# Kernel optimization log

Hardware: AMD Instinct MI355X
Metric: run time of the kernel (lower is better)

The kernel has to match this reference:

```python
import jax, jax.numpy as jnp
import numpy as np

NUM_CLUSTERS = 8
NUM_ITERS = 3
SIM_TEMP = 10.0
EPS = 1e-12  # F.normalize default eps


def _l2norm(x):
    n = jnp.linalg.norm(x, axis=-1, keepdims=True)
    return x / jnp.maximum(n, EPS)


def setup_inputs() -> dict:
    key = jax.random.key(0)
    ks = jax.random.split(key, 5)
    B, P, C = 8, 16384, 256
    F_p = jax.random.normal(ks[0], (B, P, C), dtype=jnp.float32)
    scale = 1.0 / np.sqrt(C)
    proj_w = jax.random.normal(ks[1], (C, C), dtype=jnp.float32) * scale
    proj_b = jax.random.normal(ks[2], (C,), dtype=jnp.float32) * scale
    refine_w = jax.random.normal(ks[3], (C, C), dtype=jnp.float32) * scale
    refine_b = jax.random.normal(ks[4], (C,), dtype=jnp.float32) * scale
    return {"F_p": F_p, "proj_w": proj_w, "proj_b": proj_b,
            "refine_w": refine_w, "refine_b": refine_b}


def reference(F_p, proj_w, proj_b, refine_w, refine_b):
    B, P, C = F_p.shape
    c = min(NUM_CLUSTERS, P)
    nodes = F_p @ proj_w.T + proj_b  # (B, P, C)
    # initial centers: evenly spaced node indices (torch.linspace(...).long())
    idx = jnp.asarray(np.linspace(0, P - 1, c).astype(np.int64))
    centers = nodes[:, idx, :]  # (B, c, C)
    nodes_norm = _l2norm(nodes)
    for _ in range(NUM_ITERS):
        sim = jnp.einsum('bpc,bkc->bpk', nodes_norm, _l2norm(centers))
        assignments = jnp.argmax(sim, axis=-1)  # (B, P)
        onehot = jax.nn.one_hot(assignments, c, dtype=nodes.dtype)  # (B, P, c)
        counts = jnp.maximum(onehot.sum(axis=1), 1.0)  # (B, c), clamp(min=1)
        # masked mean per cluster == segment mean via one-hot contraction
        centers = jnp.einsum('bpk,bpc->bkc', onehot, nodes) / counts[..., None]
    sim = jnp.einsum('bpc,bkc->bpk', nodes_norm, _l2norm(centers))
    weights = jax.nn.softmax(sim * SIM_TEMP, axis=-1)  # (B, P, c)
    clustered = jnp.einsum('bpk,bkc->bpc', weights, centers)
    return (clustered + F_p) @ refine_w.T + refine_b
```

## Files before the change

### kernel.cpp

```cpp
#include <hip/hip_runtime.h>
#include <hip/hip_bf16.h>
#include <cmath>

#define BB 8
#define PP 16384
#define CC 256
#define NCLUS 8
#define BPROWS (BB*PP)

typedef unsigned int uint;
typedef unsigned short ushort;
typedef __bf16 bf16x8 __attribute__((ext_vector_type(8)));
typedef float f32x16 __attribute__((ext_vector_type(16)));

__device__ __forceinline__ float bflo(uint u){ return __uint_as_float(u << 16); }
__device__ __forceinline__ float bfhi(uint u){ return __uint_as_float(u & 0xffff0000u); }
__device__ __forceinline__ ushort f2bf(float x){ __hip_bfloat16 h = __float2bfloat16(x); return *(ushort*)&h; }
__device__ __forceinline__ uint pk2(float a, float b){ return (uint)f2bf(a) | ((uint)f2bf(b) << 16); }

__global__ __launch_bounds__(256) void wcvt(const float* __restrict__ Wp,
    const float* __restrict__ Wr, ushort* __restrict__ Wpb, ushort* __restrict__ Wrb) {
  int i = blockIdx.x*256 + threadIdx.x;
  float4 a = *(const float4*)(Wp + (size_t)i*4);
  float4 b = *(const float4*)(Wr + (size_t)i*4);
  *(uint2*)(Wpb + (size_t)i*4) = make_uint2(pk2(a.x,a.y), pk2(a.z,a.w));
  *(uint2*)(Wrb + (size_t)i*4) = make_uint2(pk2(b.x,b.y), pk2(b.z,b.w));
}

template<bool PROJ>
__global__ __launch_bounds__(512) void gemm_bf16(const void* __restrict__ Av,
    const ushort* __restrict__ Wb, const float* __restrict__ bias,
    void* __restrict__ Dv, float* __restrict__ rnorm,
    const float* __restrict__ W8, const float* __restrict__ CR,
    ushort* __restrict__ fbf) {
  __shared__ __align__(16) char AlB[128*64*2];
  __shared__ __align__(16) char WlB[256*64*2];
  __shared__ float rnp[128][4];
  const int t  = threadIdx.x;
  const int p0 = blockIdx.x * 128;
  const int lane = t & 63;
  const int w  = t >> 6;
  const int wr = w >> 2, wc = w & 3;

  int aoff[2]; size_t agb[2];
  const ushort* asrc[2]; char* adst[2];
  #pragma unroll
  for (int i = 0; i < 2; ++i) {
    int S = i*512 + t, row = S >> 3, sc = S & 7;
    if constexpr (PROJ) {
      aoff[i] = row*128 + ((sc*16) ^ ((row & 7) << 4));
      agb[i]  = (size_t)(p0 + row)*CC + sc*8;
    } else {
      asrc[i] = (const ushort*)Av + (size_t)(p0 + row)*CC + ((sc ^ (row & 7)) << 3);
      adst[i] = AlB + (size_t)S*16;
    }
  }
  const ushort* wsrc[4]; char* wdst[4];
  #pragma unroll
  for (int i = 0; i < 4; ++i) {
    int S = i*512 + t, row = S >> 3, sc = S & 7;
    wsrc[i] = Wb + (size_t)row*CC + ((sc ^ (row & 7)) << 3);
    wdst[i] = WlB + (size_t)S*16;
  }
  const int arow = (wr << 6) + (lane & 31);
  const int brow = (wc << 6) + (lane & 31);
  const int kb0  = (lane >> 5) << 4;

  uint4 ra[2];
  auto LOADA = [&](int ks) {
    const float* A = (const float*)Av;
    #pragma unroll
    for (int i = 0; i < 2; ++i) {
      float4 v0 = *(const float4*)(A + agb[i] + ks*64);
      float4 v1 = *(const float4*)(A + agb[i] + ks*64 + 4);
      ra[i] = make_uint4(pk2(v0.x,v0.y), pk2(v0.z,v0.w), pk2(v1.x,v1.y), pk2(v1.z,v1.w));
    }
  };
  auto WRITEA = [&](int ks) {
    #pragma unroll
    for (int i = 0; i < 2; ++i) {
      *(uint4*)(AlB + aoff[i]) = ra[i];
      *(uint4*)(fbf + agb[i] + ks*64) = ra[i];
    }
  };
  auto STAGEA_LDS = [&](int ks) {
    #pragma unroll
    for (int i = 0; i < 2; ++i)
      __builtin_amdgcn_global_load_lds(
          (const __attribute__((address_space(1))) uint*)(asrc[i] + ks*64),
          (__attribute__((address_space(3))) uint*)adst[i], 16, 0, 0);
  };
  auto STAGEW = [&](int ks) {
    #pragma unroll
    for (int i = 0; i < 4; ++i)
      __builtin_amdgcn_global_load_lds(
          (const __attribute__((address_space(1))) uint*)(wsrc[i] + ks*64),
          (__attribute__((address_space(3))) uint*)wdst[i], 16, 0, 0);
  };

  f32x16 acc[2][2];
  #pragma unroll
  for (int fm = 0; fm < 2; ++fm)
    #pragma unroll
    for (int fn = 0; fn < 2; ++fn)
      #pragma unroll
      for (int r = 0; r < 16; ++r) acc[fm][fn][r] = 0.0f;

  if constexpr (PROJ) {
    LOADA(0); STAGEW(0); WRITEA(0);
  } else {
    STAGEA_LDS(0); STAGEW(0);
  }
  __syncthreads();

  #pragma unroll
  for (int ks = 0; ks < 4; ++ks) {
    if constexpr (PROJ) { if (ks < 3) LOADA(ks+1); }
    bf16x8 af[2][4], bg[2][4];
    #pragma unroll
    for (int fm = 0; fm < 2; ++fm)
      #pragma unroll
      for (int kq = 0; kq < 4; ++kq) {
        int row = arow + (fm << 5);
        int off = row*128 + (((kq << 5) + kb0) ^ ((row & 7) << 4));
        af[fm][kq] = *(const bf16x8*)(AlB + off);
      }
    #pragma unroll
    for (int fn = 0; fn < 2; ++fn)
      #pragma unroll
      for (int kq = 0; kq < 4; ++kq) {
        int row = brow + (fn << 5);
        int off = row*128 + (((kq << 5) + kb0) ^ ((row & 7) << 4));
        bg[fn][kq] = *(const bf16x8*)(WlB + off);
      }
    #pragma unroll
    for (int kq = 0; kq < 4; ++kq)
      #pragma unroll
      for (int fm = 0; fm < 2; ++fm)
        #pragma unroll
        for (int fn = 0; fn < 2; ++fn)
          acc[fm][fn] = __builtin_amdgcn_mfma_f32_32x32x16_bf16(
              af[fm][kq], bg[fn][kq], acc[fm][fn], 0, 0, 0);
    if (ks < 3) {
      __syncthreads();
      if constexpr (PROJ) { STAGEW(ks+1); WRITEA(ks+1); }
      else               { STAGEA_LDS(ks+1); STAGEW(ks+1); }
      __syncthreads();
    }
  }

  const int colb = (wc << 6) + (lane & 31);
  const float b0 = bias[colb], b1 = bias[colb + 32];
  float cr0[8], cr1[8];
  if constexpr (!PROJ) {
    const float* crb = CR + (size_t)(blockIdx.x >> 7)*NCLUS*CC;
    #pragma unroll
    for (int k = 0; k < 8; ++k) { cr0[k] = crb[k*CC + colb]; cr1[k] = crb[k*CC + colb + 32]; }
  }
  #pragma unroll
  for (int fm = 0; fm < 2; ++fm) {
    float rs[16];
    #pragma unroll
    for (int r = 0; r < 16; ++r) {
      int rowin = (r & 3) + ((r >> 2) << 3) + ((lane >> 5) << 2);
      size_t grow = (size_t)(p0 + (wr << 6) + (fm << 5) + rowin);
      float v0 = acc[fm][0][r] + b0;
      float v1 = acc[fm][1][r] + b1;
      if constexpr (PROJ) {
        ushort* D = (ushort*)Dv;
        D[grow*CC + colb]      = f2bf(v0);
        D[grow*CC + colb + 32] = f2bf(v1);
        rs[r] = v0*v0 + v1*v1;
      } else {
        float4 ua = *(const float4*)(W8 + grow*8);
        float4 ub = *(const float4*)(W8 + grow*8 + 4);
        v0 += ua.x*cr0[0] + ua.y*cr0[1] + ua.z*cr0[2] + ua.w*cr0[3]
            + ub.x*cr0[4] + ub.y*cr0[5] + ub.z*cr0[6] + ub.w*cr0[7];
        v1 += ua.x*cr1[0] + ua.y*cr1[1] + ua.z*cr1[2] + ua.w*cr1[3]
            + ub.x*cr1[4] + ub.y*cr1[5] + ub.z*cr1[6] + ub.w*cr1[7];
        float* D = (float*)Dv;
        D[grow*CC + colb]      = v0;
        D[grow*CC + colb + 32] = v1;
      }
    }
    if constexpr (PROJ) {
      #pragma unroll
      for (int m = 1; m < 32; m <<= 1)
        #pragma unroll
        for (int r = 0; r < 16; ++r) rs[r] += __shfl_xor(rs[r], m);
      if ((lane & 31) == 0) {
        #pragma unroll
        for (int r = 0; r < 16; ++r) {
          int rowin = (r & 3) + ((r >> 2) << 3) + ((lane >> 5) << 2);
          rnp[(wr << 6) + (fm << 5) + rowin][wc] = rs[r];
        }
      }
    }
  }
  if constexpr (PROJ) {
    __syncthreads();
    if (t < 128) {
      float s = rnp[t][0] + rnp[t][1] + rnp[t][2] + rnp[t][3];
      rnorm[p0 + t] = 1.0f / fmaxf(sqrtf(s), 1e-12f);
    }
  }
}

__global__ __launch_bounds__(256) void centers_init(const ushort* __restrict__ nbf,
    float* __restrict__ centers, ushort* __restrict__ cnormbf,
    float* __restrict__ accs, float* __restrict__ counts) {
  const int idxs[8] = {0, 2340, 4680, 7021, 9361, 11702, 14042, 16383};
  const int row = blockIdx.x;
  const int b = row >> 3, k = row & 7;
  const int t = threadIdx.x;
  float c = __uint_as_float(((uint)nbf[((size_t)b*PP + idxs[k])*CC + t]) << 16);
  centers[(size_t)row*CC + t] = c;
  float s2 = c*c;
  #pragma unroll
  for (int o = 32; o; o >>= 1) s2 += __shfl_xor(s2, o);
  __shared__ float ps[4];
  if ((t & 63) == 0) ps[t >> 6] = s2;
  __syncthreads();
  float tot = ps[0] + ps[1] + ps[2] + ps[3];
  cnormbf[(size_t)row*CC + t] = f2bf(c * (1.0f / fmaxf(sqrtf(tot), 1e-12f)));
  #pragma unroll
  for (int s = 0; s < 8; ++s) accs[((size_t)s*64 + row)*CC + t] = 0.0f;
  if (t == 0) counts[row] = 0.0f;
}

__global__ __launch_bounds__(256) void centers_finalize(float* __restrict__ accs,
    float* __restrict__ counts, ushort* __restrict__ cnormbf, float* __restrict__ centers) {
  const int row = blockIdx.x;
  const int t = threadIdx.x;
  float v = 0.0f;
  #pragma unroll
  for (int s = 0; s < 8; ++s) {
    v += accs[((size_t)s*64 + row)*CC + t];
    accs[((size_t)s*64 + row)*CC + t] = 0.0f;
  }
  float cnt = fmaxf(counts[row], 1.0f);
  float c = v / cnt;
  centers[(size_t)row*CC + t] = c;
  float s2 = c*c;
  #pragma unroll
  for (int o = 32; o; o >>= 1) s2 += __shfl_xor(s2, o);
  __shared__ float ps[4];
  if ((t & 63) == 0) ps[t >> 6] = s2;
  __syncthreads();
  float tot = ps[0] + ps[1] + ps[2] + ps[3];
  cnormbf[(size_t)row*CC + t] = f2bf(c * (1.0f / fmaxf(sqrtf(tot), 1e-12f)));
  if (t == 0) counts[row] = 0.0f;
}

__global__ __launch_bounds__(256) void cr8_compute(const float* __restrict__ centers,
    const float* __restrict__ Wr, float* __restrict__ CR) {
  __shared__ float cenL[CC];
  const int row = blockIdx.x;
  const int t = threadIdx.x;
  cenL[t] = centers[(size_t)row*CC + t];
  __syncthreads();
  float a = 0.0f;
  const float* wrow = Wr + (size_t)t*CC;
  #pragma unroll 4
  for (int j = 0; j < CC; j += 4) {
    float4 wv = *(const float4*)(wrow + j);
    float4 cv = *(const float4*)&cenL[j];
    a += cv.x*wv.x + cv.y*wv.y + cv.z*wv.z + cv.w*wv.w;
  }
  CR[(size_t)row*CC + t] = a;
}

__device__ __forceinline__ void sims_mfma(const ushort* __restrict__ nb_base,
    const ushort* __restrict__ cnb, int lane, float* s) {
  const int pcol = lane & 31;
  const int kb   = (lane >> 5) << 3;
  const ushort* arow = cnb + (size_t)(pcol & 7)*CC + kb;
  const ushort* brow = nb_base + (size_t)pcol*CC + kb;
  const bool azero = pcol >= 8;
  bf16x8 z;
  #pragma unroll
  for (int j = 0; j < 8; ++j) z[j] = (__bf16)0.0f;
  f32x16 acc;
  #pragma unroll
  for (int r = 0; r < 16; ++r) acc[r] = 0.0f;
  #pragma unroll
  for (int st = 0; st < 16; ++st) {
    bf16x8 af = *(const bf16x8*)(arow + st*16);
    if (azero) af = z;
    bf16x8 bg = *(const bf16x8*)(brow + st*16);
    acc = __builtin_amdgcn_mfma_f32_32x32x16_bf16(af, bg, acc, 0, 0, 0);
  }
  float sh[4];
  #pragma unroll
  for (int r = 0; r < 4; ++r) sh[r] = __shfl_xor(acc[r], 32);
  const bool hi = lane >= 32;
  #pragma unroll
  for (int r = 0; r < 4; ++r) {
    s[r]     = hi ? sh[r]  : acc[r];
    s[r + 4] = hi ? acc[r] : sh[r];
  }
}

__global__ __launch_bounds__(256) void assign_mfma(const ushort* __restrict__ nbf,
    const ushort* __restrict__ cnormbf, float* __restrict__ accs, float* __restrict__ counts) {
  __shared__ int assignL[128];
  __shared__ int cntL[NCLUS];
  const int t = threadIdx.x;
  const int wave = t >> 6, lane = t & 63;
  const int b = blockIdx.x >> 7;
  if (t < NCLUS) cntL[t] = 0;
  __syncthreads();
  const size_t p0w = (size_t)blockIdx.x*128 + wave*32;
  float s[8];
  sims_mfma(nbf + p0w*CC, cnormbf + (size_t)b*NCLUS*CC, lane, s);
  if (lane < 32) {
    int best = 0; float bs = s[0];
    #pragma unroll
    for (int k = 1; k < 8; ++k) if (s[k] > bs) { bs = s[k]; best = k; }
    assignL[wave*32 + lane] = best;
    atomicAdd(&cntL[best], 1);
  }
  __syncthreads();
  float a[8] = {0,0,0,0,0,0,0,0};
  const ushort* base = nbf + (size_t)blockIdx.x*128*CC;
  #pragma unroll 4
  for (int i = 0; i < 128; ++i) {
    int asg = __builtin_amdgcn_readfirstlane(assignL[i]);
    float v = __uint_as_float(((uint)base[(size_t)i*CC + t]) << 16);
    if      (asg == 0) a[0] += v;
    else if (asg == 1) a[1] += v;
    else if (asg == 2) a[2] += v;
    else if (asg == 3) a[3] += v;
    else if (asg == 4) a[4] += v;
    else if (asg == 5) a[5] += v;
    else if (asg == 6) a[6] += v;
    else               a[7] += v;
  }
  const int slot = blockIdx.x & 7;
  float* dst = accs + ((size_t)slot*BB + b)*NCLUS*CC;
  #pragma unroll
  for (int k = 0; k < 8; ++k) atomicAdd(&dst[k*CC + t], a[k]);
  if (t < NCLUS) atomicAdd(&counts[b*NCLUS + t], (float)cntL[t]);
}

__global__ __launch_bounds__(256) void fuse_w8(const ushort* __restrict__ nbf,
    const ushort* __restrict__ cnormbf, const float* __restrict__ rnorm,
    float* __restrict__ W8) {
  const int t = threadIdx.x;
  const int wave = t >> 6, lane = t & 63;
  const int b = blockIdx.x >> 7;
  const size_t p0w = (size_t)blockIdx.x*128 + wave*32;
  float s[8];
  sims_mfma(nbf + p0w*CC, cnormbf + (size_t)b*NCLUS*CC, lane, s);
  const int pcol = lane & 31;
  const float rn10 = rnorm[p0w + pcol] * 10.0f;
  float m = -1e30f;
  #pragma unroll
  for (int k = 0; k < 8; ++k) { s[k] *= rn10; m = fmaxf(m, s[k]); }
  float wgt[8], sw = 0.0f;
  #pragma unroll
  for (int k = 0; k < 8; ++k) { wgt[k] = __expf(s[k] - m); sw += wgt[k]; }
  const float inv = 1.0f / sw;
  if (lane < 32) {
    float* wp = W8 + (p0w + pcol)*8;
    *(float4*)(wp)     = make_float4(wgt[0]*inv, wgt[1]*inv, wgt[2]*inv, wgt[3]*inv);
    *(float4*)(wp + 4) = make_float4(wgt[4]*inv, wgt[5]*inv, wgt[6]*inv, wgt[7]*inv);
  }
}

extern "C" void kernel_launch(void* const* d_in, const int* in_sizes, int n_in,
                              void* d_out, int out_size, void* d_ws, size_t ws_size,
                              hipStream_t stream) {
  const float* F_p      = (const float*)d_in[0];
  const float* proj_w   = (const float*)d_in[1];
  const float* proj_b   = (const float*)d_in[2];
  const float* refine_w = (const float*)d_in[3];
  const float* refine_b = (const float*)d_in[4];
  float* out = (float*)d_out;

  char* ws = (char*)d_ws;
  ushort* nbf    = (ushort*)ws;
  ushort* fbf    = (ushort*)(ws + (size_t)BPROWS*CC*2);
  float*  rnorm  = (float*)(ws + (size_t)BPROWS*CC*4);
  float*  centers= rnorm + BPROWS;
  float*  accs   = centers + BB*NCLUS*CC;
  float*  counts = accs + 8*BB*NCLUS*CC;
  float*  CR     = counts + 64;
  ushort* cnormbf= (ushort*)(CR + BB*NCLUS*CC);
  ushort* Wpb    = cnormbf + BB*NCLUS*CC;
  ushort* Wrb    = Wpb + CC*CC;
  float*  W8     = (float*)(Wrb + CC*CC);

  wcvt<<<64, 256, 0, stream>>>(proj_w, refine_w, Wpb, Wrb);
  gemm_bf16<true><<<1024, 512, 0, stream>>>(F_p, Wpb, proj_b, nbf, rnorm, nullptr, nullptr, fbf);
  centers_init<<<64, 256, 0, stream>>>(nbf, centers, cnormbf, accs, counts);
  for (int it = 0; it < 3; ++it) {
    assign_mfma<<<1024, 256, 0, stream>>>(nbf, cnormbf, accs, counts);
    centers_finalize<<<64, 256, 0, stream>>>(accs, counts, cnormbf, centers);
  }
  fuse_w8<<<1024, 256, 0, stream>>>(nbf, cnormbf, rnorm, W8);
  cr8_compute<<<64, 256, 0, stream>>>(centers, refine_w, CR);
  gemm_bf16<false><<<1024, 512, 0, stream>>>(fbf, Wrb, refine_b, out, nullptr, W8, CR, nullptr);
}
```

Before: 285.0 us.

## Double-buffer A tile in LDS and load weight fragments directly from global

The GEMM kernel stops staging the weight tile in LDS. Each lane now reads its B fragments straight from global memory, relying on the small weight matrix being cache-resident. The A tile is double-buffered so the next k-slice can be prefetched into the alternate buffer while the current one is consumed, which removes one barrier per k-step. The trade-off is more global/L2 traffic for the weights, with uncoalesced per-lane 16-byte reads, in exchange for less LDS use and fewer syncs.

Result: slower. 334.0 us (+17.2%).

```diff
diff --git a/kernel.cpp b/kernel.cpp
--- a/kernel.cpp
+++ b/kernel.cpp
@@ -33,8 +33,7 @@
     void* __restrict__ Dv, float* __restrict__ rnorm,
     const float* __restrict__ W8, const float* __restrict__ CR,
     ushort* __restrict__ fbf) {
-  __shared__ __align__(16) char AlB[128*64*2];
-  __shared__ __align__(16) char WlB[256*64*2];
+  __shared__ __align__(16) char AlB[2][128*64*2];
   __shared__ float rnp[128][4];
   const int t  = threadIdx.x;
   const int p0 = blockIdx.x * 128;
@@ -43,7 +42,7 @@
   const int wr = w >> 2, wc = w & 3;
 
   int aoff[2]; size_t agb[2];
-  const ushort* asrc[2]; char* adst[2];
+  const ushort* asrc[2]; int adoff[2];
   #pragma unroll
   for (int i = 0; i < 2; ++i) {
     int S = i*512 + t, row = S >> 3, sc = S & 7;
@@ -51,20 +50,13 @@
       aoff[i] = row*128 + ((sc*16) ^ ((row & 7) << 4));
       agb[i]  = (size_t)(p0 + row)*CC + sc*8;
     } else {
-      asrc[i] = (const ushort*)Av + (size_t)(p0 + row)*CC + ((sc ^ (row & 7)) << 3);
-      adst[i] = AlB + (size_t)S*16;
-    }
-  }
-  const ushort* wsrc[4]; char* wdst[4];
-  #pragma unroll
-  for (int i = 0; i < 4; ++i) {
-    int S = i*512 + t, row = S >> 3, sc = S & 7;
-    wsrc[i] = Wb + (size_t)row*CC + ((sc ^ (row & 7)) << 3);
-    wdst[i] = WlB + (size_t)S*16;
+      asrc[i]  = (const ushort*)Av + (size_t)(p0 + row)*CC + ((sc ^ (row & 7)) << 3);
+      adoff[i] = S*16;
+    }
   }
   const int arow = (wr << 6) + (lane & 31);
   const int brow = (wc << 6) + (lane & 31);
-  const int kb0  = (lane >> 5) << 4;
+  const ushort* wptr = Wb + (size_t)brow*CC + ((lane >> 5) << 3);
 
   uint4 ra[2];
   auto LOADA = [&](int ks) {
@@ -76,27 +68,20 @@
       ra[i] = make_uint4(pk2(v0.x,v0.y), pk2(v0.z,v0.w), pk2(v1.x,v1.y), pk2(v1.z,v1.w));
     }
   };
-  auto WRITEA = [&](int ks) {
+  auto WRITEA = [&](int ks, char* abuf) {
     #pragma unroll
     for (int i = 0; i < 2; ++i) {
-      *(uint4*)(AlB + aoff[i]) = ra[i];
+      *(uint4*)(abuf + aoff[i]) = ra[i];
       *(uint4*)(fbf + agb[i] + ks*64) = ra[i];
     }
   };
-  auto STAGEA_LDS = [&](int ks) {
+  auto STAGEA = [&](int ks, char* abuf) {
     #pragma unroll
     for (int i = 0; i < 2; ++i)
       __builtin_amdgcn_global_load_lds(
           (const __attribute__((address_space(1))) uint*)(asrc[i] + ks*64),
-          (__attribute__((address_space(3))) uint*)adst[i], 16, 0, 0);
+          (__attribute__((address_space(3))) uint*)(abuf + adoff[i]), 16, 0, 0);
   };
-  auto STAGEW = [&](int ks) {
-    #pragma unroll
-    for (int i = 0; i < 4; ++i)
-      __builtin_amdgcn_global_load_lds(
-          (const __attribute__((address_space(1))) uint*)(wsrc[i] + ks*64),
-          (__attribute__((address_space(3))) uint*)wdst[i], 16, 0, 0);
-  };
 
   f32x16 acc[2][2];
   #pragma unroll
@@ -106,32 +91,32 @@
       #pragma unroll
       for (int r = 0; r < 16; ++r) acc[fm][fn][r] = 0.0f;
 
-  if constexpr (PROJ) {
-    LOADA(0); STAGEW(0); WRITEA(0);
-  } else {
-    STAGEA_LDS(0); STAGEW(0);
-  }
+  if constexpr (PROJ) { LOADA(0); WRITEA(0, AlB[0]); }
+  else                { STAGEA(0, AlB[0]); }
   __syncthreads();
 
   #pragma unroll
   for (int ks = 0; ks < 4; ++ks) {
-    if constexpr (PROJ) { if (ks < 3) LOADA(ks+1); }
-    bf16x8 af[2][4], bg[2][4];
+    char* cur = AlB[ks & 1];
+    char* nxt = AlB[(ks + 1) & 1];
+    if (ks < 3) {
+      if constexpr (PROJ) LOADA(ks + 1);
+      else                STAGEA(ks + 1, nxt);
+    }
+    bf16x8 bg[2][4];
+    #pragma unroll
+    for (int fn = 0; fn < 2; ++fn)
+      #pragma unroll
+      for (int kq = 0; kq < 4; ++kq)
+        bg[fn][kq] = *(const bf16x8*)(wptr + (size_t)fn*32*CC + ks*64 + kq*16);
+    bf16x8 af[2][4];
     #pragma unroll
     for (int fm = 0; fm < 2; ++fm)
       #pragma unroll
       for (int kq = 0; kq < 4; ++kq) {
         int row = arow + (fm << 5);
-        int off = row*128 + (((kq << 5) + kb0) ^ ((row & 7) << 4));
-        af[fm][kq] = *(const bf16x8*)(AlB + off);
-      }
-    #pragma unroll
-    for (int fn = 0; fn < 2; ++fn)
-      #pragma unroll
-      for (int kq = 0; kq < 4; ++kq) {
-        int row = brow + (fn << 5);
-        int off = row*128 + (((kq << 5) + kb0) ^ ((row & 7) << 4));
-        bg[fn][kq] = *(const bf16x8*)(WlB + off);
+        int off = row*128 + (((kq << 5) + ((lane >> 5) << 4)) ^ ((row & 7) << 4));
+        af[fm][kq] = *(const bf16x8*)(cur + off);
       }
     #pragma unroll
     for (int kq = 0; kq < 4; ++kq)
@@ -142,9 +127,7 @@
           acc[fm][fn] = __builtin_amdgcn_mfma_f32_32x32x16_bf16(
               af[fm][kq], bg[fn][kq], acc[fm][fn], 0, 0, 0);
     if (ks < 3) {
-      __syncthreads();
-      if constexpr (PROJ) { STAGEW(ks+1); WRITEA(ks+1); }
-      else               { STAGEA_LDS(ks+1); STAGEW(ks+1); }
+      if constexpr (PROJ) WRITEA(ks + 1, nxt);
       __syncthreads();
     }
   }
```

## Fuse softmax weight computation into refine GEMM and CR into final center update

Applied to the files above, without the earlier changes.

The separate fuse_w8 kernel is removed: the second GEMM now computes the per-row similarity softmax weights in its first four waves during the prologue and keeps them in shared memory, so the W8 buffer is never written to or read from global memory. The cr8_compute kernel is folded into the last centers_finalize launch through a template flag, and the stored float centers buffer is dropped. This removes two launches and a global round trip, but adds extra MFMA and load work to the GEMM prologue, which may delay the main loop.

After: 282.4 us. About the same (-0.9%).

```diff
diff --git a/kernel.cpp b/kernel.cpp
--- a/kernel.cpp
+++ b/kernel.cpp
@@ -14,7 +14,6 @@
 typedef float f32x16 __attribute__((ext_vector_type(16)));
 
 __device__ __forceinline__ float bflo(uint u){ return __uint_as_float(u << 16); }
-__device__ __forceinline__ float bfhi(uint u){ return __uint_as_float(u & 0xffff0000u); }
 __device__ __forceinline__ ushort f2bf(float x){ __hip_bfloat16 h = __float2bfloat16(x); return *(ushort*)&h; }
 __device__ __forceinline__ uint pk2(float a, float b){ return (uint)f2bf(a) | ((uint)f2bf(b) << 16); }
 
@@ -27,15 +26,46 @@
   *(uint2*)(Wrb + (size_t)i*4) = make_uint2(pk2(b.x,b.y), pk2(b.z,b.w));
 }
 
+__device__ __forceinline__ void sims_mfma(const ushort* __restrict__ nb_base,
+    const ushort* __restrict__ cnb, int lane, float* s) {
+  const int pcol = lane & 31;
+  const int kb   = (lane >> 5) << 3;
+  const ushort* arow = cnb + (size_t)(pcol & 7)*CC + kb;
+  const ushort* brow = nb_base + (size_t)pcol*CC + kb;
+  const bool azero = pcol >= 8;
+  bf16x8 z;
+  #pragma unroll
+  for (int j = 0; j < 8; ++j) z[j] = (__bf16)0.0f;
+  f32x16 acc;
+  #pragma unroll
+  for (int r = 0; r < 16; ++r) acc[r] = 0.0f;
+  #pragma unroll
+  for (int st = 0; st < 16; ++st) {
+    bf16x8 af = *(const bf16x8*)(arow + st*16);
+    if (azero) af = z;
+    bf16x8 bg = *(const bf16x8*)(brow + st*16);
+    acc = __builtin_amdgcn_mfma_f32_32x32x16_bf16(af, bg, acc, 0, 0, 0);
+  }
+  float sh[4];
+  #pragma unroll
+  for (int r = 0; r < 4; ++r) sh[r] = __shfl_xor(acc[r], 32);
+  const bool hi = lane >= 32;
+  #pragma unroll
+  for (int r = 0; r < 4; ++r) {
+    s[r]     = hi ? sh[r]  : acc[r];
+    s[r + 4] = hi ? acc[r] : sh[r];
+  }
+}
+
 template<bool PROJ>
 __global__ __launch_bounds__(512) void gemm_bf16(const void* __restrict__ Av,
     const ushort* __restrict__ Wb, const float* __restrict__ bias,
     void* __restrict__ Dv, float* __restrict__ rnorm,
-    const float* __restrict__ W8, const float* __restrict__ CR,
-    ushort* __restrict__ fbf) {
+    const float* __restrict__ CR, ushort* __restrict__ fbf,
+    const ushort* __restrict__ nbf, const ushort* __restrict__ cnormbf) {
   __shared__ __align__(16) char AlB[128*64*2];
   __shared__ __align__(16) char WlB[256*64*2];
-  __shared__ float rnp[128][4];
+  __shared__ __align__(16) float shr8[128][8];
   const int t  = threadIdx.x;
   const int p0 = blockIdx.x * 128;
   const int lane = t & 63;
@@ -83,7 +113,7 @@
       *(uint4*)(fbf + agb[i] + ks*64) = ra[i];
     }
   };
-  auto STAGEA_LDS = [&](int ks) {
+  auto STAGEA = [&](int ks) {
     #pragma unroll
     for (int i = 0; i < 2; ++i)
       __builtin_amdgcn_global_load_lds(
@@ -109,13 +139,32 @@
   if constexpr (PROJ) {
     LOADA(0); STAGEW(0); WRITEA(0);
   } else {
-    STAGEA_LDS(0); STAGEW(0);
+    STAGEA(0); STAGEW(0);
+    if (w < 4) {
+      const size_t p0w = (size_t)p0 + w*32;
+      float s[8];
+      sims_mfma(nbf + p0w*CC, cnormbf + (size_t)(blockIdx.x >> 7)*NCLUS*CC, lane, s);
+      const int pcol = lane & 31;
+      const float rn10 = rnorm[p0w + pcol] * 10.0f;
+      float m = -1e30f;
+      #pragma unroll
+      for (int k = 0; k < 8; ++k) { s[k] *= rn10; m = fmaxf(m, s[k]); }
+      float wgt[8], sw = 0.0f;
+      #pragma unroll
+      for (int k = 0; k < 8; ++k) { wgt[k] = __expf(s[k] - m); sw += wgt[k]; }
+      const float inv = 1.0f / sw;
+      if (lane < 32) {
+        float* wp = &shr8[w*32 + pcol][0];
+        *(float4*)(wp)     = make_float4(wgt[0]*inv, wgt[1]*inv, wgt[2]*inv, wgt[3]*inv);
+        *(float4*)(wp + 4) = make_float4(wgt[4]*inv, wgt[5]*inv, wgt[6]*inv, wgt[7]*inv);
+      }
+    }
   }
   __syncthreads();
 
   #pragma unroll
   for (int ks = 0; ks < 4; ++ks) {
-    if constexpr (PROJ) { if (ks < 3) LOADA(ks+1); }
+    if constexpr (PROJ) { if (ks < 3) LOADA(ks + 1); }
     bf16x8 af[2][4], bg[2][4];
     #pragma unroll
     for (int fm = 0; fm < 2; ++fm)
@@ -143,8 +192,8 @@
               af[fm][kq], bg[fn][kq], acc[fm][fn], 0, 0, 0);
     if (ks < 3) {
       __syncthreads();
-      if constexpr (PROJ) { STAGEW(ks+1); WRITEA(ks+1); }
-      else               { STAGEA_LDS(ks+1); STAGEW(ks+1); }
+      if constexpr (PROJ) { STAGEW(ks + 1); WRITEA(ks + 1); }
+      else                { STAGEA(ks + 1); STAGEW(ks + 1); }
       __syncthreads();
     }
   }
@@ -163,7 +212,8 @@
     #pragma unroll
     for (int r = 0; r < 16; ++r) {
       int rowin = (r & 3) + ((r >> 2) << 3) + ((lane >> 5) << 2);
-      size_t grow = (size_t)(p0 + (wr << 6) + (fm << 5) + rowin);
+      int r128  = (wr << 6) + (fm << 5) + rowin;
+      size_t grow = (size_t)(p0 + r128);
       float v0 = acc[fm][0][r] + b0;
       float v1 = acc[fm][1][r] + b1;
       if constexpr (PROJ) {
@@ -172,8 +222,8 @@
         D[grow*CC + colb + 32] = f2bf(v1);
         rs[r] = v0*v0 + v1*v1;
       } else {
-        float4 ua = *(const float4*)(W8 + grow*8);
-        float4 ub = *(const float4*)(W8 + grow*8 + 4);
+        float4 ua = *(const float4*)&shr8[r128][0];
+        float4 ub = *(const float4*)&shr8[r128][4];
         v0 += ua.x*cr0[0] + ua.y*cr0[1] + ua.z*cr0[2] + ua.w*cr0[3]
             + ub.x*cr0[4] + ub.y*cr0[5] + ub.z*cr0[6] + ub.w*cr0[7];
         v1 += ua.x*cr1[0] + ua.y*cr1[1] + ua.z*cr1[2] + ua.w*cr1[3]
@@ -192,7 +242,7 @@
         #pragma unroll
         for (int r = 0; r < 16; ++r) {
           int rowin = (r & 3) + ((r >> 2) << 3) + ((lane >> 5) << 2);
-          rnp[(wr << 6) + (fm << 5) + rowin][wc] = rs[r];
+          shr8[(wr << 6) + (fm << 5) + rowin][wc] = rs[r];
         }
       }
     }
@@ -200,21 +250,19 @@
   if constexpr (PROJ) {
     __syncthreads();
     if (t < 128) {
-      float s = rnp[t][0] + rnp[t][1] + rnp[t][2] + rnp[t][3];
+      float s = shr8[t][0] + shr8[t][1] + shr8[t][2] + shr8[t][3];
       rnorm[p0 + t] = 1.0f / fmaxf(sqrtf(s), 1e-12f);
     }
   }
 }
 
 __global__ __launch_bounds__(256) void centers_init(const ushort* __restrict__ nbf,
-    float* __restrict__ centers, ushort* __restrict__ cnormbf,
-    float* __restrict__ accs, float* __restrict__ counts) {
+    ushort* __restrict__ cnormbf, float* __restrict__ accs, float* __restrict__ counts) {
   const int idxs[8] = {0, 2340, 4680, 7021, 9361, 11702, 14042, 16383};
   const int row = blockIdx.x;
   const int b = row >> 3, k = row & 7;
   const int t = threadIdx.x;
   float c = __uint_as_float(((uint)nbf[((size_t)b*PP + idxs[k])*CC + t]) << 16);
-  centers[(size_t)row*CC + t] = c;
   float s2 = c*c;
   #pragma unroll
   for (int o = 32; o; o >>= 1) s2 += __shfl_xor(s2, o);
@@ -228,76 +276,41 @@
   if (t == 0) counts[row] = 0.0f;
 }
 
+template<bool DO_CR>
 __global__ __launch_bounds__(256) void centers_finalize(float* __restrict__ accs,
-    float* __restrict__ counts, ushort* __restrict__ cnormbf, float* __restrict__ centers) {
-  const int row = blockIdx.x;
-  const int t = threadIdx.x;
-  float v = 0.0f;
-  #pragma unroll
-  for (int s = 0; s < 8; ++s) {
-    v += accs[((size_t)s*64 + row)*CC + t];
-    accs[((size_t)s*64 + row)*CC + t] = 0.0f;
-  }
-  float cnt = fmaxf(counts[row], 1.0f);
-  float c = v / cnt;
-  centers[(size_t)row*CC + t] = c;
-  float s2 = c*c;
-  #pragma unroll
-  for (int o = 32; o; o >>= 1) s2 += __shfl_xor(s2, o);
-  __shared__ float ps[4];
-  if ((t & 63) == 0) ps[t >> 6] = s2;
-  __syncthreads();
-  float tot = ps[0] + ps[1] + ps[2] + ps[3];
-  cnormbf[(size_t)row*CC + t] = f2bf(c * (1.0f / fmaxf(sqrtf(tot), 1e-12f)));
-  if (t == 0) counts[row] = 0.0f;
-}
-
-__global__ __launch_bounds__(256) void cr8_compute(const float* __restrict__ centers,
+    float* __restrict__ counts, ushort* __restrict__ cnormbf,
     const float* __restrict__ Wr, float* __restrict__ CR) {
   __shared__ float cenL[CC];
   const int row = blockIdx.x;
   const int t = threadIdx.x;
-  cenL[t] = centers[(size_t)row*CC + t];
-  __syncthreads();
-  float a = 0.0f;
-  const float* wrow = Wr + (size_t)t*CC;
-  #pragma unroll 4
-  for (int j = 0; j < CC; j += 4) {
-    float4 wv = *(const float4*)(wrow + j);
-    float4 cv = *(const float4*)&cenL[j];
-    a += cv.x*wv.x + cv.y*wv.y + cv.z*wv.z + cv.w*wv.w;
-  }
-  CR[(size_t)row*CC + t] = a;
-}
-
-__device__ __forceinline__ void sims_mfma(const ushort* __restrict__ nb_base,
-    const ushort* __restrict__ cnb, int lane, float* s) {
-  const int pcol = lane & 31;
-  const int kb   = (lane >> 5) << 3;
-  const ushort* arow = cnb + (size_t)(pcol & 7)*CC + kb;
-  const ushort* brow = nb_base + (size_t)pcol*CC + kb;
-  const bool azero = pcol >= 8;
-  bf16x8 z;
-  #pragma unroll
-  for (int j = 0; j < 8; ++j) z[j] = (__bf16)0.0f;
-  f32x16 acc;
-  #pragma unroll
-  for (int r = 0; r < 16; ++r) acc[r] = 0.0f;
-  #pragma unroll
-  for (int st = 0; st < 16; ++st) {
-    bf16x8 af = *(const bf16x8*)(arow + st*16);
-    if (azero) af = z;
-    bf16x8 bg = *(const bf16x8*)(brow + st*16);
-    acc = __builtin_amdgcn_mfma_f32_32x32x16_bf16(af, bg, acc, 0, 0, 0);
-  }
-  float sh[4];
-  #pragma unroll
-  for (int r = 0; r < 4; ++r) sh[r] = __shfl_xor(acc[r], 32);
-  const bool hi = lane >= 32;
-  #pragma unroll
-  for (int r = 0; r < 4; ++r) {
-    s[r]     = hi ? sh[r]  : acc[r];
-    s[r + 4] = hi ? acc[r] : sh[r];
+  float v = 0.0f;
+  #pragma unroll
+  for (int s = 0; s < 8; ++s) {
+    v += accs[((size_t)s*64 + row)*CC + t];
+    accs[((size_t)s*64 + row)*CC + t] = 0.0f;
+  }
+  float cnt = fmaxf(counts[row], 1.0f);
+  float c = v / cnt;
+  if constexpr (DO_CR) cenL[t] = c;
+  float s2 = c*c;
+  #pragma unroll
+  for (int o = 32; o; o >>= 1) s2 += __shfl_xor(s2, o);
+  __shared__ float ps[4];
+  if ((t & 63) == 0) ps[t >> 6] = s2;
+  __syncthreads();
+  float tot = ps[0] + ps[1] + ps[2] + ps[3];
+  cnormbf[(size_t)row*CC + t] = f2bf(c * (1.0f / fmaxf(sqrtf(tot), 1e-12f)));
+  if (t == 0) counts[row] = 0.0f;
+  if constexpr (DO_CR) {
+    float a = 0.0f;
+    const float* wrow = Wr + (size_t)t*CC;
+    #pragma unroll 4
+    for (int j = 0; j < CC; j += 4) {
+      float4 wv = *(const float4*)(wrow + j);
+      float4 cv = *(const float4*)&cenL[j];
+      a += cv.x*wv.x + cv.y*wv.y + cv.z*wv.z + cv.w*wv.w;
+    }
+    CR[(size_t)row*CC + t] = a;
   }
 }
 
@@ -343,31 +356,6 @@
   if (t < NCLUS) atomicAdd(&counts[b*NCLUS + t], (float)cntL[t]);
 }
 
-__global__ __launch_bounds__(256) void fuse_w8(const ushort* __restrict__ nbf,
-    const ushort* __restrict__ cnormbf, const float* __restrict__ rnorm,
-    float* __restrict__ W8) {
-  const int t = threadIdx.x;
-  const int wave = t >> 6, lane = t & 63;
-  const int b = blockIdx.x >> 7;
-  const size_t p0w = (size_t)blockIdx.x*128 + wave*32;
-  float s[8];
-  sims_mfma(nbf + p0w*CC, cnormbf + (size_t)b*NCLUS*CC, lane, s);
-  const int pcol = lane & 31;
-  const float rn10 = rnorm[p0w + pcol] * 10.0f;
-  float m = -1e30f;
-  #pragma unroll
-  for (int k = 0; k < 8; ++k) { s[k] *= rn10; m = fmaxf(m, s[k]); }
-  float wgt[8], sw = 0.0f;
-  #pragma unroll
-  for (int k = 0; k < 8; ++k) { wgt[k] = __expf(s[k] - m); sw += wgt[k]; }
-  const float inv = 1.0f / sw;
-  if (lane < 32) {
-    float* wp = W8 + (p0w + pcol)*8;
-    *(float4*)(wp)     = make_float4(wgt[0]*inv, wgt[1]*inv, wgt[2]*inv, wgt[3]*inv);
-    *(float4*)(wp + 4) = make_float4(wgt[4]*inv, wgt[5]*inv, wgt[6]*inv, wgt[7]*inv);
-  }
-}
-
 extern "C" void kernel_launch(void* const* d_in, const int* in_sizes, int n_in,
                               void* d_out, int out_size, void* d_ws, size_t ws_size,
                               hipStream_t stream) {
@@ -382,23 +370,22 @@
   ushort* nbf    = (ushort*)ws;
   ushort* fbf    = (ushort*)(ws + (size_t)BPROWS*CC*2);
   float*  rnorm  = (float*)(ws + (size_t)BPROWS*CC*4);
-  float*  centers= rnorm + BPROWS;
-  float*  accs   = centers + BB*NCLUS*CC;
+  float*  accs   = rnorm + BPROWS;
   float*  counts = accs + 8*BB*NCLUS*CC;
   float*  CR     = counts + 64;
   ushort* cnormbf= (ushort*)(CR + BB*NCLUS*CC);
   ushort* Wpb    = cnormbf + BB*NCLUS*CC;
   ushort* Wrb    = Wpb + CC*CC;
-  float*  W8     = (float*)(Wrb + CC*CC);
 
   wcvt<<<64, 256, 0, stream>>>(proj_w, refine_w, Wpb, Wrb);
-  gemm_bf16<true><<<1024, 512, 0, stream>>>(F_p, Wpb, proj_b, nbf, rnorm, nullptr, nullptr, fbf);
-  centers_init<<<64, 256, 0, stream>>>(nbf, centers, cnormbf, accs, counts);
+  gemm_bf16<true><<<1024, 512, 0, stream>>>(F_p, Wpb, proj_b, nbf, rnorm,
+                                            nullptr, fbf, nullptr, nullptr);
+  centers_init<<<64, 256, 0, stream>>>(nbf, cnormbf, accs, counts);
   for (int it = 0; it < 3; ++it) {
     assign_mfma<<<1024, 256, 0, stream>>>(nbf, cnormbf, accs, counts);
-    centers_finalize<<<64, 256, 0, stream>>>(accs, counts, cnormbf, centers);
-  }
-  fuse_w8<<<1024, 256, 0, stream>>>(nbf, cnormbf, rnorm, W8);
-  cr8_compute<<<64, 256, 0, stream>>>(centers, refine_w, CR);
-  gemm_bf16<false><<<1024, 512, 0, stream>>>(fbf, Wrb, refine_b, out, nullptr, W8, CR, nullptr);
-}
+    if (it < 2) centers_finalize<false><<<64, 256, 0, stream>>>(accs, counts, cnormbf, nullptr, nullptr);
+    else        centers_finalize<true ><<<64, 256, 0, stream>>>(accs, counts, cnormbf, refine_w, CR);
+  }
+  gemm_bf16<false><<<1024, 512, 0, stream>>>(fbf, Wrb, refine_b, out, rnorm,
+                                             CR, nullptr, nbf, cnormbf);
+}
```
